# Optimization experiments

Hardware: AMD Instinct MI355X
Metric: run time of the kernel (lower is better)

Reference implementation:

```python
import jax, jax.numpy as jnp
import numpy as np

N_T, N_Q, N_NODE, D, CH, K, NB, B = 32, 256, 8192, 128, 32, 16, 8, 4
LIN_MULT = 1.0
ANG_MULT = float(np.sqrt(2.0))
GAMMA = 4.0
RBF_C = jnp.linspace(0.0, 3.0, NB)


def quat_apply(q, v):
    # rotate v by unit quaternion q (w,x,y,z)
    w, u = q[..., :1], q[..., 1:]
    uv = jnp.cross(u, v)
    return v + 2.0 * (w * uv + jnp.cross(u, uv))


def quat_invert(q):
    return q * jnp.array([1.0, -1.0, -1.0, -1.0], dtype=q.dtype)


def split_irreps(f):
    # '32x0e + 32x1e': first CH scalars, then CH 3-vectors
    s = f[..., :CH]
    v = f[..., CH:].reshape(f.shape[:-1] + (CH, 3))
    return s, v


def dtp(s, v, t, u, w_path, W_scal, W_vec):
    # Separable (depthwise, uvu) fully-connected tensor product:
    # per-channel CG paths, then e3nn-style linear mixing within each irrep type.
    p_ss = w_path[0] * s * t                          # 0e x 0e -> 0e   [N,CH]
    p_dot = w_path[1] * jnp.sum(v * u, -1)            # 1e x 1e -> 0e   [N,CH]
    p_su = w_path[2][:, None] * s[..., None] * u      # 0e x 1e -> 1e   [N,CH,3]
    p_vt = w_path[3][:, None] * v * t[..., None]      # 1e x 0e -> 1e   [N,CH,3]
    p_x = w_path[4][:, None] * jnp.cross(v, u)        # 1e x 1e -> 1e   [N,CH,3]
    scal = jax.nn.silu(jnp.concatenate([p_ss, p_dot], -1) @ W_scal)          # [N,1]
    vec = jnp.einsum('ncd,co->nod', jnp.concatenate([p_su, p_vt, p_x], -2), W_vec)  # [N,CH,3]
    return jnp.concatenate([scal, vec.reshape(vec.shape[0], CH * 3)], -1)    # [N,1+3*CH]


def extract_field(qc, qb, node_feature, node_coord, nb, time_emb, W_ext, W_rbf, W_time):
    # gather-based key extractor: K nearest same-batch nodes, radial-basis weighted sum
    d2 = jnp.sum((qc[:, None, :] - node_coord[None, :, :]) ** 2, -1)   # [NTQ, N_NODE]
    d2 = jnp.where(qb[:, None] == nb[None, :], d2, 1e9)
    neg, idx = jax.lax.top_k(-d2, K)
    d = jnp.sqrt(jnp.maximum(-neg, 1e-12))                              # [NTQ, K]
    feats = node_feature[idx] @ W_ext                                   # [NTQ, K, D]
    rbf = jnp.exp(-GAMMA * (d[..., None] - RBF_C) ** 2)                 # [NTQ, K, NB]
    field = jnp.sum((rbf @ W_rbf) * feats, 1)                           # [NTQ, D]
    return field * (1.0 + time_emb @ W_time)                            # FiLM by time embedding


def setup_inputs() -> dict:
    key = jax.random.key(0)
    ks = jax.random.split(key, 16)
    Traw = jax.random.normal(ks[0], (N_T, 7), jnp.float32)
    q = Traw[:, :4] / jnp.linalg.norm(Traw[:, :4], axis=-1, keepdims=True)
    T = jnp.concatenate([q, Traw[:, 4:]], -1)
    return {
        'T': T,
        'query_weight': jax.random.uniform(ks[1], (N_Q,), jnp.float32),
        'query_feature': jax.random.normal(ks[2], (N_Q, D), jnp.float32),
        'query_coord': jax.random.normal(ks[3], (N_Q, 3), jnp.float32),
        'node_feature': jax.random.normal(ks[4], (N_NODE, D), jnp.float32),
        'node_coord': jax.random.normal(ks[5], (N_NODE, 3), jnp.float32),
        'time_emb': jax.random.normal(ks[6], (1, D), jnp.float32),
        'W_ext': jax.random.normal(ks[7], (D, D), jnp.float32) / np.sqrt(D),
        'W_rbf': jax.random.normal(ks[8], (NB, D), jnp.float32) / np.sqrt(NB),
        'W_time': jax.random.normal(ks[9], (D, D), jnp.float32) / np.sqrt(D),
        'w_path_lin': jax.random.normal(ks[10], (5, CH), jnp.float32),
        'W_scal_lin': jax.random.normal(ks[11], (2 * CH, 1), jnp.float32) / np.sqrt(2 * CH),
        'W_vec_lin': jax.random.normal(ks[12], (3 * CH, CH), jnp.float32) / np.sqrt(3 * CH),
        'w_path_ang': jax.random.normal(ks[13], (5, CH), jnp.float32),
        'W_scal_ang': jax.random.normal(ks[14], (2 * CH, 1), jnp.float32) / np.sqrt(2 * CH),
        'W_vec_ang': jax.random.normal(ks[15], (3 * CH, CH), jnp.float32) / np.sqrt(3 * CH),
        'query_batch': jax.random.randint(jax.random.fold_in(key, 1), (N_Q,), 0, B),
        'node_batch': jnp.sort(jax.random.randint(jax.random.fold_in(key, 2), (N_NODE,), 0, B)),
    }


def reference(T, query_weight, query_feature, query_coord, node_feature, node_coord, time_emb, W_ext, W_rbf, W_time, w_path_lin, W_scal_lin, W_vec_lin, w_path_ang, W_scal_ang, W_vec_ang, query_batch, node_batch):
    q, X = T[:, :4], T[:, 4:]
    # transform query coords by each pose
    qc = quat_apply(q[:, None, :], query_coord[None, :, :]) + X[:, None, :]   # [N_T,N_Q,3]
    # quaternion-equivariant feature transform: rotate every 1e channel
    s0, v0 = split_irreps(query_feature)                                      # [N_Q,CH],[N_Q,CH,3]
    v_rot = quat_apply(q[:, None, None, :], v0[None])                         # [N_T,N_Q,CH,3]
    qs = jnp.broadcast_to(s0[None], (N_T, N_Q, CH)).reshape(N_T * N_Q, CH)
    qv = v_rot.reshape(N_T * N_Q, CH, 3)
    qb = jnp.broadcast_to(query_batch[None], (N_T, N_Q)).reshape(-1)
    field = extract_field(qc.reshape(N_T * N_Q, 3), qb, node_feature, node_coord, node_batch, time_emb, W_ext, W_rbf, W_time)
    t, u = split_irreps(field)
    lin = dtp(qs, qv, t, u, w_path_lin, W_scal_lin, W_vec_lin)[:, 1:]         # drop 1x0e
    ang = dtp(qs, qv, t, u, w_path_ang, W_scal_ang, W_vec_ang)[:, 1:]
    lin_vel = lin.reshape(N_T, N_Q, CH, 3).mean(-2)                           # [N_T,N_Q,3]
    ang_spin = ang.reshape(N_T, N_Q, CH, 3).mean(-2)
    qinv = quat_invert(q)[:, None, :]
    lin_vel = quat_apply(qinv, lin_vel)
    ang_spin = quat_apply(qinv, ang_spin)
    ang_orbital = jnp.cross(jnp.broadcast_to(query_coord[None], lin_vel.shape), lin_vel)
    lin_out = jnp.einsum('q,tqi->ti', query_weight, lin_vel) / LIN_MULT
    ang_out = jnp.einsum('q,tqi->ti', query_weight, ang_orbital) / LIN_MULT + jnp.einsum('q,tqi->ti', query_weight, ang_spin) / ANG_MULT
    return ang_out, lin_out
```

## Files before the change

kernel.cpp:

```cpp
#include <hip/hip_runtime.h>
#include <math.h>

#define NT 32
#define NQ 256
#define NN 8192
#define DD 128
#define CHN 32
#define KK 16
#define NBB 8
#define NBATCH 4
#define CAP 128
#define TFUSE 4

__device__ float g_NF2[NN * DD];
__device__ float g_gate[DD];
__device__ float g_coef[192];
__device__ int   g_bstart[NBATCH];
__device__ int   g_bend[NBATCH];
__device__ float g_part[NT * NQ * 6];

__device__ __forceinline__ void quat_rot(float w, float x, float y, float z,
                                         float v0, float v1, float v2,
                                         float& r0, float& r1, float& r2) {
  float uv0 = y * v2 - z * v1;
  float uv1 = z * v0 - x * v2;
  float uv2 = x * v1 - y * v0;
  float uuv0 = y * uv2 - z * uv1;
  float uuv1 = z * uv0 - x * uv2;
  float uuv2 = x * uv1 - y * uv0;
  r0 = v0 + 2.0f * (w * uv0 + uuv0);
  r1 = v1 + 2.0f * (w * uv1 + uuv1);
  r2 = v2 + 2.0f * (w * uv2 + uuv2);
}

__device__ __forceinline__ void quat_rot_d(double w, double x, double y, double z,
                                           double v0, double v1, double v2,
                                           double& r0, double& r1, double& r2) {
  double uv0 = y * v2 - z * v1;
  double uv1 = z * v0 - x * v2;
  double uv2 = x * v1 - y * v0;
  double uuv0 = y * uv2 - z * uv1;
  double uuv1 = z * uv0 - x * uv2;
  double uuv2 = x * uv1 - y * uv0;
  r0 = v0 + 2.0 * (w * uv0 + uuv0);
  r1 = v1 + 2.0 * (w * uv1 + uuv1);
  r2 = v2 + 2.0 * (w * uv2 + uuv2);
}

__global__ __launch_bounds__(256) void prep_kernel(
    const float* __restrict__ nf, const float* __restrict__ W_ext,
    const int* __restrict__ node_batch, const float* __restrict__ time_emb,
    const float* __restrict__ W_time,
    const float* __restrict__ w_path_lin, const float* __restrict__ W_vec_lin,
    const float* __restrict__ w_path_ang, const float* __restrict__ W_vec_ang) {
  int tid = threadIdx.x;
  if (blockIdx.x == 512) {
    if (tid < NBATCH) { g_bstart[tid] = 0; g_bend[tid] = 0; }
    __syncthreads();
    for (int i = tid; i < NN; i += 256) {
      int v = node_batch[i];
      if (i == 0 || node_batch[i - 1] != v) g_bstart[v] = i;
      if (i == NN - 1 || node_batch[i + 1] != v) g_bend[v] = i + 1;
    }
    if (tid < DD) {
      float g = 0.0f;
      for (int d = 0; d < DD; d++) g += time_emb[d] * W_time[d * DD + tid];
      g_gate[tid] = 1.0f + g;
    }
    if (tid < 192) {
      int arr = tid >> 5, c = tid & 31;
      int path = (arr >= 3) ? (arr - 3) : arr;
      const float* Wv = (arr < 3) ? W_vec_lin : W_vec_ang;
      const float* wp = (arr < 3) ? w_path_lin : w_path_ang;
      float s = 0.0f;
      for (int o = 0; o < CHN; o++) s += Wv[(path * CHN + c) * CHN + o];
      g_coef[tid] = wp[(2 + path) * CHN + c] * (s * (1.0f / 32.0f));
    }
    return;
  }
  int gid = blockIdx.x * 256 + tid;
  int j = gid & (DD - 1);
  int n0 = (gid >> 7) * 8;
  n0 = __builtin_amdgcn_readfirstlane(n0);
  float acc[8] = {0, 0, 0, 0, 0, 0, 0, 0};
  const float* nfr = nf + (long)n0 * DD;
#pragma unroll 4
  for (int d = 0; d < DD; d++) {
    float w = W_ext[d * DD + j];
#pragma unroll
    for (int rr = 0; rr < 8; rr++) acc[rr] += nfr[rr * DD + d] * w;
  }
#pragma unroll
  for (int rr = 0; rr < 8; rr++) g_NF2[(n0 + rr) * DD + j] = acc[rr];
}

__global__ __launch_bounds__(256) void main_kernel(
    const float* __restrict__ Tm,
    const float* __restrict__ qwgt,
    const float* __restrict__ qfeat,
    const float* __restrict__ qcoord,
    const float* __restrict__ ncoord,
    const float* __restrict__ W_rbf,
    const int* __restrict__ qbatch) {
  __shared__ int s_cidx[4][TFUSE][CAP];
  __shared__ float s_kd[4][KK];
  __shared__ int s_kidx[4][KK];
  __shared__ float s_rbf[4][KK * NBB];
  __shared__ float s_field[4][DD];

  int lane = threadIdx.x & 63;
  int wid = threadIdx.x >> 6;
  int w = blockIdx.x * 4 + wid;
  int q = w >> 3;
  int tg = w & 7;

  float c0 = qcoord[q * 3 + 0], c1 = qcoord[q * 3 + 1], c2 = qcoord[q * 3 + 2];
  int b = qbatch[q];
  int sBeg = g_bstart[b], sEnd = g_bend[b];

  float pf0[TFUSE], pf1[TFUSE], pf2[TFUSE];
#pragma unroll
  for (int tt = 0; tt < TFUSE; tt++) {
    int t = tg * TFUSE + tt;
    double dr0, dr1, dr2;
    quat_rot_d((double)Tm[t * 7 + 0], (double)Tm[t * 7 + 1],
               (double)Tm[t * 7 + 2], (double)Tm[t * 7 + 3],
               (double)c0, (double)c1, (double)c2, dr0, dr1, dr2);
    pf0[tt] = (float)(dr0 + (double)Tm[t * 7 + 4]);
    pf1[tt] = (float)(dr1 + (double)Tm[t * 7 + 5]);
    pf2[tt] = (float)(dr2 + (double)Tm[t * 7 + 6]);
  }

  float lm[TFUSE];
#pragma unroll
  for (int tt = 0; tt < TFUSE; tt++) lm[tt] = 3.0e38f;
  for (int i = sBeg + lane; i < sEnd; i += 256) {
#pragma unroll
    for (int sub = 0; sub < 4; sub++) {
      int ii = i + (sub << 6);
      if (ii < sEnd) {
        float x = ncoord[3 * ii + 0];
        float y = ncoord[3 * ii + 1];
        float z = ncoord[3 * ii + 2];
#pragma unroll
        for (int tt = 0; tt < TFUSE; tt++) {
          float dx = pf0[tt] - x, dy = pf1[tt] - y, dz = pf2[tt] - z;
          lm[tt] = fminf(lm[tt], dx * dx + dy * dy + dz * dz);
        }
      }
    }
  }

  float thrv[TFUSE];
#pragma unroll
  for (int tt = 0; tt < TFUSE; tt++) {
    float v = lm[tt];
#pragma unroll
    for (int k = 2; k <= 64; k <<= 1) {
#pragma unroll
      for (int j = k >> 1; j > 0; j >>= 1) {
        float o = __shfl_xor(v, j, 64);
        bool keep_min = (((lane & j) == 0) == ((lane & k) == 0));
        v = keep_min ? fminf(v, o) : fmaxf(v, o);
      }
    }
    thrv[tt] = __shfl(v, 15, 64) + 1.0e-3f;
  }

  int base[TFUSE];
#pragma unroll
  for (int tt = 0; tt < TFUSE; tt++) base[tt] = 0;
  for (int i0 = sBeg; i0 < sEnd; i0 += 64) {
    int i = i0 + lane;
    bool inb = (i < sEnd);
    float x = 0.0f, y = 0.0f, z = 0.0f;
    if (inb) {
      x = ncoord[3 * i + 0];
      y = ncoord[3 * i + 1];
      z = ncoord[3 * i + 2];
    }
#pragma unroll
    for (int tt = 0; tt < TFUSE; tt++) {
      bool pred = false;
      if (inb) {
        float dx = pf0[tt] - x, dy = pf1[tt] - y, dz = pf2[tt] - z;
        pred = (dx * dx + dy * dy + dz * dz) <= thrv[tt];
      }
      unsigned long long bal = __ballot(pred);
      int pre = __popcll(bal & ((1ull << lane) - 1ull));
      if (pred) {
        int pos = base[tt] + pre;
        if (pos < CAP) s_cidx[wid][tt][pos] = i;
      }
      base[tt] += __popcll(bal);
    }
  }

  float sc = 0, w0 = 0, w1 = 0, w2 = 0;
  if (lane < CHN) {
    sc = qfeat[q * DD + lane];
    w0 = qfeat[q * DD + CHN + 3 * lane + 0];
    w1 = qfeat[q * DD + CHN + 3 * lane + 1];
    w2 = qfeat[q * DD + CHN + 3 * lane + 2];
  }
  float wq = qwgt[q];

  for (int tt = 0; tt < TFUSE; tt++) {
    int t = tg * TFUSE + tt;
    float Qw = Tm[t * 7 + 0], Qx = Tm[t * 7 + 1], Qy = Tm[t * 7 + 2], Qz = Tm[t * 7 + 3];
    float Xx = Tm[t * 7 + 4], Xy = Tm[t * 7 + 5], Xz = Tm[t * 7 + 6];
    double dr0, dr1, dr2;
    quat_rot_d((double)Qw, (double)Qx, (double)Qy, (double)Qz,
               (double)c0, (double)c1, (double)c2, dr0, dr1, dr2);
    double p0 = dr0 + (double)Xx, p1 = dr1 + (double)Xy, p2 = dr2 + (double)Xz;
    float qr0 = (float)dr0, qr1 = (float)dr1, qr2 = (float)dr2;
    int ncand = base[tt] < CAP ? base[tt] : CAP;

    if (ncand <= 64) {
      unsigned long long key = ~0ull;
      if (lane < ncand) {
        int idx = s_cidx[wid][tt][lane];
        double dx = p0 - (double)ncoord[3 * idx + 0];
        double dy = p1 - (double)ncoord[3 * idx + 1];
        double dz = p2 - (double)ncoord[3 * idx + 2];
        double d2 = dx * dx + dy * dy + dz * dz;
        key = (((unsigned long long)__double_as_longlong(d2)) & ~0x1FFFull) |
              (unsigned long long)idx;
      }
#pragma unroll
      for (int k = 2; k <= 64; k <<= 1) {
#pragma unroll
        for (int j = k >> 1; j > 0; j >>= 1) {
          unsigned long long o = __shfl_xor(key, j, 64);
          bool keep_min = (((lane & j) == 0) == ((lane & k) == 0));
          unsigned long long mn = o < key ? o : key;
          unsigned long long mx = o < key ? key : o;
          key = keep_min ? mn : mx;
        }
      }
      if (lane < KK) {
        double d2m = __longlong_as_double((long long)(key & ~0x1FFFull));
        s_kidx[wid][lane] = (int)(key & 0x1FFFull);
        s_kd[wid][lane] = (float)sqrt(fmax(d2m, 1.0e-12));
      }
    } else {
      unsigned long long key[2];
#pragma unroll
      for (int s = 0; s < 2; s++) {
        int pos = lane + 64 * s;
        if (pos < ncand) {
          int idx = s_cidx[wid][tt][pos];
          double dx = p0 - (double)ncoord[3 * idx + 0];
          double dy = p1 - (double)ncoord[3 * idx + 1];
          double dz = p2 - (double)ncoord[3 * idx + 2];
          double d2 = dx * dx + dy * dy + dz * dz;
          key[s] = (((unsigned long long)__double_as_longlong(d2)) & ~0x1FFFull) |
                   (unsigned long long)idx;
        } else {
          key[s] = ~0ull;
        }
      }
      for (int r = 0; r < KK; r++) {
        unsigned long long kmin = key[0] < key[1] ? key[0] : key[1];
#pragma unroll
        for (int off = 32; off > 0; off >>= 1) {
          unsigned long long o = __shfl_xor(kmin, off, 64);
          kmin = (o < kmin) ? o : kmin;
        }
        if (lane == 0) {
          double d2m = __longlong_as_double((long long)(kmin & ~0x1FFFull));
          s_kidx[wid][r] = (int)(kmin & 0x1FFFull);
          s_kd[wid][r] = (float)sqrt(fmax(d2m, 1.0e-12));
        }
#pragma unroll
        for (int s = 0; s < 2; s++)
          if (key[s] == kmin) key[s] = ~0ull;
      }
    }

    for (int kr = lane; kr < KK * NBB; kr += 64) {
      int k = kr >> 3, r = kr & 7;
      float d = s_kd[wid][k];
      float cc = (3.0f / 7.0f) * (float)r;
      float diff = d - cc;
      s_rbf[wid][kr] = expf(-4.0f * diff * diff);
    }

    for (int jj = 0; jj < 2; jj++) {
      int j = lane + 64 * jj;
      float wr[NBB];
#pragma unroll
      for (int r = 0; r < NBB; r++) wr[r] = W_rbf[r * DD + j];
      float acc = 0.0f;
#pragma unroll
      for (int k = 0; k < KK; k++) {
        float rw = 0.0f;
#pragma unroll
        for (int r = 0; r < NBB; r++) rw += s_rbf[wid][k * NBB + r] * wr[r];
        acc += rw * g_NF2[s_kidx[wid][k] * DD + j];
      }
      s_field[wid][j] = acc * g_gate[j];
    }

    float r0 = 0, r1 = 0, r2 = 0, r3 = 0, r4 = 0, r5 = 0;
    if (lane < CHN) {
      int c = lane;
      float tF = s_field[wid][c];
      float u0 = s_field[wid][CHN + 3 * c + 0];
      float u1 = s_field[wid][CHN + 3 * c + 1];
      float u2 = s_field[wid][CHN + 3 * c + 2];
      float v0r, v1r, v2r;
      quat_rot(Qw, Qx, Qy, Qz, w0, w1, w2, v0r, v1r, v2r);
      float cx0 = v1r * u2 - v2r * u1;
      float cx1 = v2r * u0 - v0r * u2;
      float cx2 = v0r * u1 - v1r * u0;
      float Al = g_coef[c], Bl = g_coef[32 + c], Cl = g_coef[64 + c];
      float Aa = g_coef[96 + c], Ba = g_coef[128 + c], Ca = g_coef[160 + c];
      float su = Al * sc, bt = Bl * tF;
      r0 = su * u0 + bt * v0r + Cl * cx0;
      r1 = su * u1 + bt * v1r + Cl * cx1;
      r2 = su * u2 + bt * v2r + Cl * cx2;
      float sa = Aa * sc, ba = Ba * tF;
      r3 = sa * u0 + ba * v0r + Ca * cx0;
      r4 = sa * u1 + ba * v1r + Ca * cx1;
      r5 = sa * u2 + ba * v2r + Ca * cx2;
    }
#pragma unroll
    for (int off = 32; off > 0; off >>= 1) {
      r0 += __shfl_xor(r0, off, 64);
      r1 += __shfl_xor(r1, off, 64);
      r2 += __shfl_xor(r2, off, 64);
      r3 += __shfl_xor(r3, off, 64);
      r4 += __shfl_xor(r4, off, 64);
      r5 += __shfl_xor(r5, off, 64);
    }
    if (lane == 0) {
      float o0 = qr1 * r2 - qr2 * r1;
      float o1 = qr2 * r0 - qr0 * r2;
      float o2 = qr0 * r1 - qr1 * r0;
      const float IA = 0.70710678118654752f;
      int pbase = (t * NQ + q) * 6;
      g_part[pbase + 0] = wq * r0;
      g_part[pbase + 1] = wq * r1;
      g_part[pbase + 2] = wq * r2;
      g_part[pbase + 3] = wq * (o0 + r3 * IA);
      g_part[pbase + 4] = wq * (o1 + r4 * IA);
      g_part[pbase + 5] = wq * (o2 + r5 * IA);
    }
  }
}

__global__ __launch_bounds__(256) void reduce_kernel(const float* __restrict__ Tm,
                                                     float* __restrict__ out) {
  __shared__ float s_sum[4][6];
  int t = blockIdx.x;
  int lane = threadIdx.x & 63;
  int wid = threadIdx.x >> 6;
  int q = threadIdx.x;
  float v[6];
#pragma unroll
  for (int c = 0; c < 6; c++) v[c] = g_part[(t * NQ + q) * 6 + c];
#pragma unroll
  for (int off = 32; off > 0; off >>= 1) {
#pragma unroll
    for (int c = 0; c < 6; c++) v[c] += __shfl_xor(v[c], off, 64);
  }
  if (lane == 0) {
#pragma unroll
    for (int c = 0; c < 6; c++) s_sum[wid][c] = v[c];
  }
  __syncthreads();
  if (threadIdx.x == 0) {
    float sL0 = 0, sL1 = 0, sL2 = 0, sA0 = 0, sA1 = 0, sA2 = 0;
#pragma unroll
    for (int ww = 0; ww < 4; ww++) {
      sL0 += s_sum[ww][0]; sL1 += s_sum[ww][1]; sL2 += s_sum[ww][2];
      sA0 += s_sum[ww][3]; sA1 += s_sum[ww][4]; sA2 += s_sum[ww][5];
    }
    float Qw = Tm[t * 7 + 0], Qx = -Tm[t * 7 + 1], Qy = -Tm[t * 7 + 2], Qz = -Tm[t * 7 + 3];
    float a0, a1, a2, l0, l1, l2;
    quat_rot(Qw, Qx, Qy, Qz, sA0, sA1, sA2, a0, a1, a2);
    quat_rot(Qw, Qx, Qy, Qz, sL0, sL1, sL2, l0, l1, l2);
    out[t * 3 + 0] = a0;
    out[t * 3 + 1] = a1;
    out[t * 3 + 2] = a2;
    out[NT * 3 + t * 3 + 0] = l0;
    out[NT * 3 + t * 3 + 1] = l1;
    out[NT * 3 + t * 3 + 2] = l2;
  }
}

extern "C" void kernel_launch(void* const* d_in, const int* in_sizes, int n_in,
                              void* d_out, int out_size, void* d_ws, size_t ws_size,
                              hipStream_t stream) {
  const float* T      = (const float*)d_in[0];
  const float* qwgt   = (const float*)d_in[1];
  const float* qfeat  = (const float*)d_in[2];
  const float* qcoord = (const float*)d_in[3];
  const float* nfeat  = (const float*)d_in[4];
  const float* ncoord = (const float*)d_in[5];
  const float* temb   = (const float*)d_in[6];
  const float* W_ext  = (const float*)d_in[7];
  const float* W_rbf  = (const float*)d_in[8];
  const float* W_time = (const float*)d_in[9];
  const float* wp_lin = (const float*)d_in[10];
  const float* Wv_lin = (const float*)d_in[12];
  const float* wp_ang = (const float*)d_in[13];
  const float* Wv_ang = (const float*)d_in[15];
  const int* qbatch   = (const int*)d_in[16];
  const int* nbatch   = (const int*)d_in[17];
  float* out = (float*)d_out;

  prep_kernel<<<513, 256, 0, stream>>>(nfeat, W_ext, nbatch, temb, W_time,
                                       wp_lin, Wv_lin, wp_ang, Wv_ang);
  main_kernel<<<512, 256, 0, stream>>>(T, qwgt, qfeat, qcoord, ncoord, W_rbf, qbatch);
  reduce_kernel<<<NT, 256, 0, stream>>>(T, out);
}
```

Before: 166.7 us.

## Split main kernel into kNN select and field/TP epilogue kernels

Divides the fused main kernel into a selection kernel that writes the K nearest indices and distances to global buffers, and a separate epilogue kernel with one wave per (t,q) pair that gathers features, builds the field and evaluates the tensor product. The epilogue now runs across 2048 blocks instead of looping over four time steps serially per wave. The aim is more parallelism and lower register and LDS pressure in each phase, at the cost of an extra launch and a global round trip for the neighbor lists.

```diff
diff --git a/kernel.cpp b/kernel.cpp
--- a/kernel.cpp
+++ b/kernel.cpp
@@ -17,6 +17,8 @@
 __device__ float g_coef[192];
 __device__ int   g_bstart[NBATCH];
 __device__ int   g_bend[NBATCH];
+__device__ int   g_kidx[NT * NQ * KK];
+__device__ float g_kd[NT * NQ * KK];
 __device__ float g_part[NT * NQ * 6];
 
 __device__ __forceinline__ void quat_rot(float w, float x, float y, float z,
@@ -94,19 +96,12 @@
   for (int rr = 0; rr < 8; rr++) g_NF2[(n0 + rr) * DD + j] = acc[rr];
 }
 
-__global__ __launch_bounds__(256) void main_kernel(
+__global__ __launch_bounds__(256) void select_kernel(
     const float* __restrict__ Tm,
-    const float* __restrict__ qwgt,
-    const float* __restrict__ qfeat,
     const float* __restrict__ qcoord,
     const float* __restrict__ ncoord,
-    const float* __restrict__ W_rbf,
     const int* __restrict__ qbatch) {
   __shared__ int s_cidx[4][TFUSE][CAP];
-  __shared__ float s_kd[4][KK];
-  __shared__ int s_kidx[4][KK];
-  __shared__ float s_rbf[4][KK * NBB];
-  __shared__ float s_field[4][DD];
 
   int lane = threadIdx.x & 63;
   int wid = threadIdx.x >> 6;
@@ -196,25 +191,17 @@
     }
   }
 
-  float sc = 0, w0 = 0, w1 = 0, w2 = 0;
-  if (lane < CHN) {
-    sc = qfeat[q * DD + lane];
-    w0 = qfeat[q * DD + CHN + 3 * lane + 0];
-    w1 = qfeat[q * DD + CHN + 3 * lane + 1];
-    w2 = qfeat[q * DD + CHN + 3 * lane + 2];
-  }
-  float wq = qwgt[q];
-
   for (int tt = 0; tt < TFUSE; tt++) {
     int t = tg * TFUSE + tt;
-    float Qw = Tm[t * 7 + 0], Qx = Tm[t * 7 + 1], Qy = Tm[t * 7 + 2], Qz = Tm[t * 7 + 3];
-    float Xx = Tm[t * 7 + 4], Xy = Tm[t * 7 + 5], Xz = Tm[t * 7 + 6];
     double dr0, dr1, dr2;
-    quat_rot_d((double)Qw, (double)Qx, (double)Qy, (double)Qz,
+    quat_rot_d((double)Tm[t * 7 + 0], (double)Tm[t * 7 + 1],
+               (double)Tm[t * 7 + 2], (double)Tm[t * 7 + 3],
                (double)c0, (double)c1, (double)c2, dr0, dr1, dr2);
-    double p0 = dr0 + (double)Xx, p1 = dr1 + (double)Xy, p2 = dr2 + (double)Xz;
-    float qr0 = (float)dr0, qr1 = (float)dr1, qr2 = (float)dr2;
+    double p0 = dr0 + (double)Tm[t * 7 + 4];
+    double p1 = dr1 + (double)Tm[t * 7 + 5];
+    double p2 = dr2 + (double)Tm[t * 7 + 6];
     int ncand = base[tt] < CAP ? base[tt] : CAP;
+    int obase = (t * NQ + q) * KK;
 
     if (ncand <= 64) {
       unsigned long long key = ~0ull;
@@ -240,8 +227,8 @@
       }
       if (lane < KK) {
         double d2m = __longlong_as_double((long long)(key & ~0x1FFFull));
-        s_kidx[wid][lane] = (int)(key & 0x1FFFull);
-        s_kd[wid][lane] = (float)sqrt(fmax(d2m, 1.0e-12));
+        g_kidx[obase + lane] = (int)(key & 0x1FFFull);
+        g_kd[obase + lane] = (float)sqrt(fmax(d2m, 1.0e-12));
       }
     } else {
       unsigned long long key[2];
@@ -269,84 +256,119 @@
         }
         if (lane == 0) {
           double d2m = __longlong_as_double((long long)(kmin & ~0x1FFFull));
-          s_kidx[wid][r] = (int)(kmin & 0x1FFFull);
-          s_kd[wid][r] = (float)sqrt(fmax(d2m, 1.0e-12));
+          g_kidx[obase + r] = (int)(kmin & 0x1FFFull);
+          g_kd[obase + r] = (float)sqrt(fmax(d2m, 1.0e-12));
         }
 #pragma unroll
         for (int s = 0; s < 2; s++)
           if (key[s] == kmin) key[s] = ~0ull;
       }
     }
-
-    for (int kr = lane; kr < KK * NBB; kr += 64) {
-      int k = kr >> 3, r = kr & 7;
-      float d = s_kd[wid][k];
-      float cc = (3.0f / 7.0f) * (float)r;
-      float diff = d - cc;
-      s_rbf[wid][kr] = expf(-4.0f * diff * diff);
-    }
-
-    for (int jj = 0; jj < 2; jj++) {
-      int j = lane + 64 * jj;
-      float wr[NBB];
-#pragma unroll
-      for (int r = 0; r < NBB; r++) wr[r] = W_rbf[r * DD + j];
-      float acc = 0.0f;
-#pragma unroll
-      for (int k = 0; k < KK; k++) {
-        float rw = 0.0f;
-#pragma unroll
-        for (int r = 0; r < NBB; r++) rw += s_rbf[wid][k * NBB + r] * wr[r];
-        acc += rw * g_NF2[s_kidx[wid][k] * DD + j];
-      }
-      s_field[wid][j] = acc * g_gate[j];
-    }
-
-    float r0 = 0, r1 = 0, r2 = 0, r3 = 0, r4 = 0, r5 = 0;
-    if (lane < CHN) {
-      int c = lane;
-      float tF = s_field[wid][c];
-      float u0 = s_field[wid][CHN + 3 * c + 0];
-      float u1 = s_field[wid][CHN + 3 * c + 1];
-      float u2 = s_field[wid][CHN + 3 * c + 2];
-      float v0r, v1r, v2r;
-      quat_rot(Qw, Qx, Qy, Qz, w0, w1, w2, v0r, v1r, v2r);
-      float cx0 = v1r * u2 - v2r * u1;
-      float cx1 = v2r * u0 - v0r * u2;
-      float cx2 = v0r * u1 - v1r * u0;
-      float Al = g_coef[c], Bl = g_coef[32 + c], Cl = g_coef[64 + c];
-      float Aa = g_coef[96 + c], Ba = g_coef[128 + c], Ca = g_coef[160 + c];
-      float su = Al * sc, bt = Bl * tF;
-      r0 = su * u0 + bt * v0r + Cl * cx0;
-      r1 = su * u1 + bt * v1r + Cl * cx1;
-      r2 = su * u2 + bt * v2r + Cl * cx2;
-      float sa = Aa * sc, ba = Ba * tF;
-      r3 = sa * u0 + ba * v0r + Ca * cx0;
-      r4 = sa * u1 + ba * v1r + Ca * cx1;
-      r5 = sa * u2 + ba * v2r + Ca * cx2;
-    }
-#pragma unroll
-    for (int off = 32; off > 0; off >>= 1) {
-      r0 += __shfl_xor(r0, off, 64);
-      r1 += __shfl_xor(r1, off, 64);
-      r2 += __shfl_xor(r2, off, 64);
-      r3 += __shfl_xor(r3, off, 64);
-      r4 += __shfl_xor(r4, off, 64);
-      r5 += __shfl_xor(r5, off, 64);
-    }
-    if (lane == 0) {
-      float o0 = qr1 * r2 - qr2 * r1;
-      float o1 = qr2 * r0 - qr0 * r2;
-      float o2 = qr0 * r1 - qr1 * r0;
-      const float IA = 0.70710678118654752f;
-      int pbase = (t * NQ + q) * 6;
-      g_part[pbase + 0] = wq * r0;
-      g_part[pbase + 1] = wq * r1;
-      g_part[pbase + 2] = wq * r2;
-      g_part[pbase + 3] = wq * (o0 + r3 * IA);
-      g_part[pbase + 4] = wq * (o1 + r4 * IA);
-      g_part[pbase + 5] = wq * (o2 + r5 * IA);
-    }
+  }
+}
+
+__global__ __launch_bounds__(256) void epi_kernel(
+    const float* __restrict__ Tm,
+    const float* __restrict__ qwgt,
+    const float* __restrict__ qfeat,
+    const float* __restrict__ qcoord,
+    const float* __restrict__ W_rbf) {
+  __shared__ float s_kd[4][KK];
+  __shared__ int s_kidx[4][KK];
+  __shared__ float s_rbf[4][KK * NBB];
+  __shared__ float s_field[4][DD];
+
+  int lane = threadIdx.x & 63;
+  int wid = threadIdx.x >> 6;
+  int m = blockIdx.x * 4 + wid;
+  int t = m >> 8, q = m & (NQ - 1);
+  int obase = m * KK;
+
+  float Qw = Tm[t * 7 + 0], Qx = Tm[t * 7 + 1], Qy = Tm[t * 7 + 2], Qz = Tm[t * 7 + 3];
+  float c0 = qcoord[q * 3 + 0], c1 = qcoord[q * 3 + 1], c2 = qcoord[q * 3 + 2];
+  double dr0, dr1, dr2;
+  quat_rot_d((double)Qw, (double)Qx, (double)Qy, (double)Qz,
+             (double)c0, (double)c1, (double)c2, dr0, dr1, dr2);
+  float qr0 = (float)dr0, qr1 = (float)dr1, qr2 = (float)dr2;
+
+  if (lane < KK) {
+    s_kidx[wid][lane] = g_kidx[obase + lane];
+    s_kd[wid][lane] = g_kd[obase + lane];
+  }
+
+  for (int kr = lane; kr < KK * NBB; kr += 64) {
+    int k = kr >> 3, r = kr & 7;
+    float d = s_kd[wid][k];
+    float cc = (3.0f / 7.0f) * (float)r;
+    float diff = d - cc;
+    s_rbf[wid][kr] = expf(-4.0f * diff * diff);
+  }
+
+  for (int jj = 0; jj < 2; jj++) {
+    int j = lane + 64 * jj;
+    float wr[NBB];
+#pragma unroll
+    for (int r = 0; r < NBB; r++) wr[r] = W_rbf[r * DD + j];
+    float acc = 0.0f;
+#pragma unroll
+    for (int k = 0; k < KK; k++) {
+      float rw = 0.0f;
+#pragma unroll
+      for (int r = 0; r < NBB; r++) rw += s_rbf[wid][k * NBB + r] * wr[r];
+      acc += rw * g_NF2[s_kidx[wid][k] * DD + j];
+    }
+    s_field[wid][j] = acc * g_gate[j];
+  }
+
+  float r0 = 0, r1 = 0, r2 = 0, r3 = 0, r4 = 0, r5 = 0;
+  if (lane < CHN) {
+    int c = lane;
+    float tF = s_field[wid][c];
+    float u0 = s_field[wid][CHN + 3 * c + 0];
+    float u1 = s_field[wid][CHN + 3 * c + 1];
+    float u2 = s_field[wid][CHN + 3 * c + 2];
+    float sc = qfeat[q * DD + c];
+    float w0 = qfeat[q * DD + CHN + 3 * c + 0];
+    float w1 = qfeat[q * DD + CHN + 3 * c + 1];
+    float w2 = qfeat[q * DD + CHN + 3 * c + 2];
+    float v0r, v1r, v2r;
+    quat_rot(Qw, Qx, Qy, Qz, w0, w1, w2, v0r, v1r, v2r);
+    float cx0 = v1r * u2 - v2r * u1;
+    float cx1 = v2r * u0 - v0r * u2;
+    float cx2 = v0r * u1 - v1r * u0;
+    float Al = g_coef[c], Bl = g_coef[32 + c], Cl = g_coef[64 + c];
+    float Aa = g_coef[96 + c], Ba = g_coef[128 + c], Ca = g_coef[160 + c];
+    float su = Al * sc, bt = Bl * tF;
+    r0 = su * u0 + bt * v0r + Cl * cx0;
+    r1 = su * u1 + bt * v1r + Cl * cx1;
+    r2 = su * u2 + bt * v2r + Cl * cx2;
+    float sa = Aa * sc, ba = Ba * tF;
+    r3 = sa * u0 + ba * v0r + Ca * cx0;
+    r4 = sa * u1 + ba * v1r + Ca * cx1;
+    r5 = sa * u2 + ba * v2r + Ca * cx2;
+  }
+#pragma unroll
+  for (int off = 32; off > 0; off >>= 1) {
+    r0 += __shfl_xor(r0, off, 64);
+    r1 += __shfl_xor(r1, off, 64);
+    r2 += __shfl_xor(r2, off, 64);
+    r3 += __shfl_xor(r3, off, 64);
+    r4 += __shfl_xor(r4, off, 64);
+    r5 += __shfl_xor(r5, off, 64);
+  }
+  if (lane == 0) {
+    float wq = qwgt[q];
+    float o0 = qr1 * r2 - qr2 * r1;
+    float o1 = qr2 * r0 - qr0 * r2;
+    float o2 = qr0 * r1 - qr1 * r0;
+    const float IA = 0.70710678118654752f;
+    int pbase = m * 6;
+    g_part[pbase + 0] = wq * r0;
+    g_part[pbase + 1] = wq * r1;
+    g_part[pbase + 2] = wq * r2;
+    g_part[pbase + 3] = wq * (o0 + r3 * IA);
+    g_part[pbase + 4] = wq * (o1 + r4 * IA);
+    g_part[pbase + 5] = wq * (o2 + r5 * IA);
   }
 }
 
@@ -413,6 +435,7 @@
 
   prep_kernel<<<513, 256, 0, stream>>>(nfeat, W_ext, nbatch, temb, W_time,
                                        wp_lin, Wv_lin, wp_ang, Wv_ang);
-  main_kernel<<<512, 256, 0, stream>>>(T, qwgt, qfeat, qcoord, ncoord, W_rbf, qbatch);
+  select_kernel<<<512, 256, 0, stream>>>(T, qcoord, ncoord, qbatch);
+  epi_kernel<<<(NT * NQ) / 4, 256, 0, stream>>>(T, qwgt, qfeat, qcoord, W_rbf);
   reduce_kernel<<<NT, 256, 0, stream>>>(T, out);
 }
```

Measured after the change: 165.8 us. About the same (-0.5%).
